# Kernel tuning notes

Hardware: AMD Instinct MI355X
Metric: run time of the kernel (lower is better)

The kernel has to match this reference:

```python
import jax, jax.numpy as jnp
import numpy as np

D = 256          # input_dim (node embedding dim)
ATT_TIMES = 2
ATT_NUM = 2
DIN = D * ATT_NUM  # NTN input dim = 512
F = 16           # feature_map_dim


def setup_inputs() -> dict:
    key = jax.random.key(0)
    ks = jax.random.split(key, 10)
    x1 = jax.random.normal(ks[0], (120000, D), dtype=jnp.float32)
    x2 = jax.random.normal(ks[1], (100000, D), dtype=jnp.float32)
    # attention weight (glorot)
    W0 = jax.random.normal(ks[2], (D, D), dtype=jnp.float32) * (2.0 / (D + D)) ** 0.5
    # NTN params
    V = jax.random.normal(ks[3], (F, 2 * DIN), dtype=jnp.float32) * (2.0 / (F + 2 * DIN)) ** 0.5
    W = jax.random.normal(ks[4], (F, DIN, DIN), dtype=jnp.float32) * (2.0 / (DIN + DIN)) ** 0.5
    b = jax.random.normal(ks[5], (F,), dtype=jnp.float32)
    # projection MLP 16->8->4->2->1, torch Linear weights are (out, in)
    P0 = jax.random.normal(ks[6], (8, 16), dtype=jnp.float32) * (2.0 / (8 + 16)) ** 0.5
    P1 = jax.random.normal(ks[7], (4, 8), dtype=jnp.float32) * (2.0 / (4 + 8)) ** 0.5
    P2 = jax.random.normal(ks[8], (2, 4), dtype=jnp.float32) * (2.0 / (2 + 4)) ** 0.5
    P3 = jax.random.normal(ks[9], (1, 2), dtype=jnp.float32) * (2.0 / (1 + 2)) ** 0.5
    return {"x1": x1, "x2": x2, "W0": W0, "V": V, "W": W, "b": b,
            "P0": P0, "P1": P1, "P2": P2, "P3": P3}


def _attention(x, W0):
    # x: (N, D) -> (1, D*ATT_NUM) graph embedding.
    outs = []
    for _ in range(ATT_NUM):  # 'dot' style: same params each head (eye W), kept for faithfulness
        cur = x
        out = None
        for _ in range(ATT_TIMES):
            temp = jnp.mean(cur, axis=0, keepdims=True)          # (1, D)
            h_avg = jnp.tanh(temp @ W0)                          # att_weight=True
            att = jax.nn.sigmoid(cur @ h_avg.T)                  # (N, 1), W=eye in 'dot' style
            out = att.T @ cur                                    # (1, D)
            cur = cur * att
        outs.append(out)
    return jnp.concatenate(outs, axis=1)                         # (1, DIN)


def _ntn(g1, g2, V, W, b):
    # g1, g2: (1, DIN). Fused bilinear over all F feature maps.
    concat = jnp.concatenate([g1, g2], axis=1)                   # (1, 2*DIN)
    v_term = concat @ V.T                                        # (1, F)
    w_term = jnp.einsum('nd,fde,me->nf', g1, W, g2)              # (1, F)
    return jax.nn.sigmoid(v_term + w_term + b)                   # inneract = sigmoid


def reference(x1, x2, W0, V, W, b, P0, P1, P2, P3):
    g1 = _attention(x1, W0)
    g2 = _attention(x2, W0)
    x = _ntn(g1, g2, V, W, b)                                    # (1, F), branch 'an'
    for P in (P0, P1, P2, P3):                                   # Linear(no bias) + Sigmoid
        x = jax.nn.sigmoid(x @ P.T)
    return x                                                     # (1, 1)
```

## Files before the change

### kernel.cpp

```cpp
#include <hip/hip_runtime.h>
#include <math.h>

#define DD 256
#define REPS 8

#define OFF_SUMREP 0
#define OFF_H1P    4096
#define OFF_S1REP  4608
#define OFF_H2P    8704
#define OFF_OREP   9216
#define OFF_O      13312
#define OFF_WTREP  13824
#define WS_FLOATS  13952

__device__ __forceinline__ float sigmoidf_(float x) { return 1.0f / (1.0f + __expf(-x)); }
__device__ __forceinline__ float dot4(float4 a, float4 b) {
    return a.x * b.x + a.y * b.y + a.z * b.z + a.w * b.w;
}
__device__ __forceinline__ void fma4(float4& acc, float s, float4 v) {
    acc.x += s * v.x; acc.y += s * v.y; acc.z += s * v.z; acc.w += s * v.w;
}
__device__ __forceinline__ float wave_sum(float v) {
#pragma unroll
    for (int off = 32; off; off >>= 1) v += __shfl_xor(v, off, 64);
    return v;
}

__global__ void k_zero(float* __restrict__ ws) {
    int i = blockIdx.x * 256 + threadIdx.x;
    if (i < WS_FLOATS) ws[i] = 0.0f;
}

__device__ __forceinline__ void block_reduce_atomic(float4 acc, int t, float* dst_base) {
    __shared__ float4 lds[256];
    lds[t] = acc;
    __syncthreads();
    if (t < 64) {
        float4 s = lds[t];
        float4 a = lds[t + 64], c = lds[t + 128], d = lds[t + 192];
        s.x += a.x + c.x + d.x; s.y += a.y + c.y + d.y;
        s.z += a.z + c.z + d.z; s.w += a.w + c.w + d.w;
        float* dst = dst_base + t * 4;
        atomicAdd(dst + 0, s.x); atomicAdd(dst + 1, s.y);
        atomicAdd(dst + 2, s.z); atomicAdd(dst + 3, s.w);
    }
}

__global__ void __launch_bounds__(256, 8)
k_mean(const float* __restrict__ x1, const float* __restrict__ x2,
       int N1, int N2, float* __restrict__ ws) {
    int b = blockIdx.x, t = threadIdx.x;
    int inp = b >> 10;
    int bl = b & 1023;
    const float4* x = (const float4*)(inp ? x2 : x1);
    int N = inp ? N2 : N1;
    int chunk = (N + 1023) >> 10;
    int start = bl * chunk;
    int end = min(start + chunk, N);
    int lane = t & 63, w = t >> 6;
    float4 a0 = make_float4(0.f, 0.f, 0.f, 0.f), a1 = a0;
    int r = start + w;
    for (; r + 12 < end; r += 16) {
        const float4* p = x + (size_t)r * 64 + lane;
        float4 v0 = p[0], v1 = p[256], v2 = p[512], v3 = p[768];
        a0.x += v0.x + v1.x; a0.y += v0.y + v1.y; a0.z += v0.z + v1.z; a0.w += v0.w + v1.w;
        a1.x += v2.x + v3.x; a1.y += v2.y + v3.y; a1.z += v2.z + v3.z; a1.w += v2.w + v3.w;
    }
    for (; r < end; r += 4) {
        float4 v = x[(size_t)r * 64 + lane];
        a0.x += v.x; a0.y += v.y; a0.z += v.z; a0.w += v.w;
    }
    a0.x += a1.x; a0.y += a1.y; a0.z += a1.z; a0.w += a1.w;
    block_reduce_atomic(a0, t, ws + OFF_SUMREP + inp * (REPS * 256) + (bl & (REPS - 1)) * 256);
}

__global__ void k_hpart(const float* __restrict__ W0, float* __restrict__ ws,
                        int srcOff, int dstOff, int N1, int N2) {
    int inp = blockIdx.x >> 4, g = blockIdx.x & 15;
    int t = threadIdx.x;
    __shared__ float temp[16];
    if (t < 16) {
        const float* src = ws + srcOff + inp * (REPS * 256) + g * 16 + t;
        float s = 0.f;
#pragma unroll
        for (int r = 0; r < REPS; r++) s += src[r * 256];
        temp[t] = s * (1.0f / (float)(inp ? N2 : N1));
    }
    __syncthreads();
    float p = 0.f;
#pragma unroll
    for (int j = 0; j < 16; j++) p += temp[j] * W0[(g * 16 + j) * 256 + t];
    atomicAdd(ws + dstOff + inp * 256 + t, p);
}

__global__ void __launch_bounds__(256, 8)
k_att1(const float* __restrict__ x1, const float* __restrict__ x2,
       int N1, int N2, float* __restrict__ ws) {
    int b = blockIdx.x, t = threadIdx.x;
    int inp = b >> 10;
    int bl = b & 1023;
    const float4* x = (const float4*)(inp ? x2 : x1);
    int N = inp ? N2 : N1;
    int chunk = (N + 1023) >> 10;
    int start = bl * chunk;
    int end = min(start + chunk, N);
    int lane = t & 63, w = t >> 6;
    float4 hp = ((const float4*)(ws + OFF_H1P + inp * 256))[lane];
    float4 h1 = make_float4(tanhf(hp.x), tanhf(hp.y), tanhf(hp.z), tanhf(hp.w));
    float4 acc = make_float4(0.f, 0.f, 0.f, 0.f);
    int r = start + w;
    for (; r + 12 < end; r += 16) {
        const float4* p = x + (size_t)r * 64 + lane;
        float4 v0 = p[0], v1 = p[256], v2 = p[512], v3 = p[768];
        float d0 = dot4(v0, h1), d1 = dot4(v1, h1), d2 = dot4(v2, h1), d3 = dot4(v3, h1);
#pragma unroll
        for (int off = 32; off; off >>= 1) {
            d0 += __shfl_xor(d0, off, 64); d1 += __shfl_xor(d1, off, 64);
            d2 += __shfl_xor(d2, off, 64); d3 += __shfl_xor(d3, off, 64);
        }
        fma4(acc, sigmoidf_(d0), v0); fma4(acc, sigmoidf_(d1), v1);
        fma4(acc, sigmoidf_(d2), v2); fma4(acc, sigmoidf_(d3), v3);
    }
    for (; r < end; r += 4) {
        float4 v = x[(size_t)r * 64 + lane];
        float d = wave_sum(dot4(v, h1));
        fma4(acc, sigmoidf_(d), v);
    }
    block_reduce_atomic(acc, t, ws + OFF_S1REP + inp * (REPS * 256) + (bl & (REPS - 1)) * 256);
}

__global__ void __launch_bounds__(256, 8)
k_att2(const float* __restrict__ x1, const float* __restrict__ x2,
       int N1, int N2, float* __restrict__ ws) {
    int b = blockIdx.x, t = threadIdx.x;
    int inp = b >> 10;
    int bl = b & 1023;
    const float4* x = (const float4*)(inp ? x2 : x1);
    int N = inp ? N2 : N1;
    int chunk = (N + 1023) >> 10;
    int start = bl * chunk;
    int end = min(start + chunk, N);
    int lane = t & 63, w = t >> 6;
    float4 hp1 = ((const float4*)(ws + OFF_H1P + inp * 256))[lane];
    float4 hp2 = ((const float4*)(ws + OFF_H2P + inp * 256))[lane];
    float4 h1 = make_float4(tanhf(hp1.x), tanhf(hp1.y), tanhf(hp1.z), tanhf(hp1.w));
    float4 h2 = make_float4(tanhf(hp2.x), tanhf(hp2.y), tanhf(hp2.z), tanhf(hp2.w));
    float4 acc = make_float4(0.f, 0.f, 0.f, 0.f);
    int r = start + w;
    for (; r + 12 < end; r += 16) {
        const float4* p = x + (size_t)r * 64 + lane;
        float4 v0 = p[0], v1 = p[256], v2 = p[512], v3 = p[768];
        float d0 = dot4(v0, h1), d1 = dot4(v1, h1), d2 = dot4(v2, h1), d3 = dot4(v3, h1);
        float e0 = dot4(v0, h2), e1 = dot4(v1, h2), e2 = dot4(v2, h2), e3 = dot4(v3, h2);
#pragma unroll
        for (int off = 32; off; off >>= 1) {
            d0 += __shfl_xor(d0, off, 64); e0 += __shfl_xor(e0, off, 64);
            d1 += __shfl_xor(d1, off, 64); e1 += __shfl_xor(e1, off, 64);
            d2 += __shfl_xor(d2, off, 64); e2 += __shfl_xor(e2, off, 64);
            d3 += __shfl_xor(d3, off, 64); e3 += __shfl_xor(e3, off, 64);
        }
        float a1_0 = sigmoidf_(d0), a1_1 = sigmoidf_(d1), a1_2 = sigmoidf_(d2), a1_3 = sigmoidf_(d3);
        fma4(acc, a1_0 * sigmoidf_(a1_0 * e0), v0);
        fma4(acc, a1_1 * sigmoidf_(a1_1 * e1), v1);
        fma4(acc, a1_2 * sigmoidf_(a1_2 * e2), v2);
        fma4(acc, a1_3 * sigmoidf_(a1_3 * e3), v3);
    }
    for (; r < end; r += 4) {
        float4 v = x[(size_t)r * 64 + lane];
        float d = dot4(v, h1), e = dot4(v, h2);
#pragma unroll
        for (int off = 32; off; off >>= 1) {
            d += __shfl_xor(d, off, 64); e += __shfl_xor(e, off, 64);
        }
        float a1 = sigmoidf_(d);
        fma4(acc, a1 * sigmoidf_(a1 * e), v);
    }
    block_reduce_atomic(acc, t, ws + OFF_OREP + inp * (REPS * 256) + (bl & (REPS - 1)) * 256);
}

__global__ void k_comb(float* __restrict__ ws) {
    int t = threadIdx.x;
    int inp = t >> 8, c = t & 255;
    float s = 0.f;
#pragma unroll
    for (int r = 0; r < REPS; r++) s += ws[OFF_OREP + inp * (REPS * 256) + r * 256 + c];
    ws[OFF_O + t] = s;
}

__global__ void __launch_bounds__(256, 8)
k_ntn(const float* __restrict__ W, float* __restrict__ ws) {
    int b = blockIdx.x, t = threadIdx.x;
    int lane = t & 63, w = t >> 6;
    const float* o1 = ws + OFF_O;
    float4 o2f = ((const float4*)(ws + OFF_O + 256))[lane];
    int f = b >> 5;
    int r0 = b * 16 + w;
    const float4* W4 = (const float4*)W;
    float p0, p1, p2, p3;
    {
        const float4* q0 = W4 + (size_t)r0 * 128 + lane;
        float4 a0 = q0[0],   c0 = q0[64];
        float4 a1 = q0[512], c1 = q0[576];
        float4 a2 = q0[1024], c2 = q0[1088];
        float4 a3 = q0[1536], c3 = q0[1600];
        p0 = (a0.x + c0.x) * o2f.x + (a0.y + c0.y) * o2f.y + (a0.z + c0.z) * o2f.z + (a0.w + c0.w) * o2f.w;
        p1 = (a1.x + c1.x) * o2f.x + (a1.y + c1.y) * o2f.y + (a1.z + c1.z) * o2f.z + (a1.w + c1.w) * o2f.w;
        p2 = (a2.x + c2.x) * o2f.x + (a2.y + c2.y) * o2f.y + (a2.z + c2.z) * o2f.z + (a2.w + c2.w) * o2f.w;
        p3 = (a3.x + c3.x) * o2f.x + (a3.y + c3.y) * o2f.y + (a3.z + c3.z) * o2f.z + (a3.w + c3.w) * o2f.w;
    }
#pragma unroll
    for (int off = 32; off; off >>= 1) {
        p0 += __shfl_xor(p0, off, 64); p1 += __shfl_xor(p1, off, 64);
        p2 += __shfl_xor(p2, off, 64); p3 += __shfl_xor(p3, off, 64);
    }
    if (lane == 0) {
        float* dst = ws + OFF_WTREP + (b & (REPS - 1)) * 16 + f;
        int d = r0 & 511;
        atomicAdd(dst, o1[d & 255] * p0
                     + o1[(d + 4) & 255] * p1
                     + o1[(d + 8) & 255] * p2
                     + o1[(d + 12) & 255] * p3);
    }
}

__global__ void k_final(const float* __restrict__ V, const float* __restrict__ bb,
                        const float* __restrict__ P0, const float* __restrict__ P1,
                        const float* __restrict__ P2, const float* __restrict__ P3,
                        float* __restrict__ ws, float* __restrict__ out) {
    int t = threadIdx.x;
    const float* o = ws + OFF_O;
    int f = t >> 4, j = t & 15;
    float p = 0.f;
    for (int k = j; k < 1024; k += 16) {
        float cv = (k < 512) ? o[k & 255] : o[256 + (k & 255)];
        p += cv * V[f * 1024 + k];
    }
    __shared__ float red[256];
    __shared__ float sv[16];
    red[t] = p;
    __syncthreads();
    if (t < 16) {
        float v = 0.f;
#pragma unroll
        for (int q = 0; q < 16; q++) v += red[t * 16 + q];
        float wt = 0.f;
#pragma unroll
        for (int r = 0; r < REPS; r++) wt += ws[OFF_WTREP + r * 16 + t];
        sv[t] = sigmoidf_(v + wt + bb[t]);
    }
    __syncthreads();
    if (t == 0) {
        float y0[8], y1[4], y2[2];
#pragma unroll
        for (int i = 0; i < 8; i++) {
            float s = 0.f;
            for (int k = 0; k < 16; k++) s += P0[i * 16 + k] * sv[k];
            y0[i] = sigmoidf_(s);
        }
#pragma unroll
        for (int i = 0; i < 4; i++) {
            float s = 0.f;
            for (int k = 0; k < 8; k++) s += P1[i * 8 + k] * y0[k];
            y1[i] = sigmoidf_(s);
        }
#pragma unroll
        for (int i = 0; i < 2; i++) {
            float s = 0.f;
            for (int k = 0; k < 4; k++) s += P2[i * 4 + k] * y1[k];
            y2[i] = sigmoidf_(s);
        }
        out[0] = sigmoidf_(P3[0] * y2[0] + P3[1] * y2[1]);
    }
}

extern "C" void kernel_launch(void* const* d_in, const int* in_sizes, int n_in,
                              void* d_out, int out_size, void* d_ws, size_t ws_size,
                              hipStream_t stream) {
    const float* x1 = (const float*)d_in[0];
    const float* x2 = (const float*)d_in[1];
    const float* W0 = (const float*)d_in[2];
    const float* V  = (const float*)d_in[3];
    const float* W  = (const float*)d_in[4];
    const float* b  = (const float*)d_in[5];
    const float* P0 = (const float*)d_in[6];
    const float* P1 = (const float*)d_in[7];
    const float* P2 = (const float*)d_in[8];
    const float* P3 = (const float*)d_in[9];
    float* ws  = (float*)d_ws;
    float* out = (float*)d_out;
    int N1 = in_sizes[0] / DD;
    int N2 = in_sizes[1] / DD;

    k_zero  <<<55,   256, 0, stream>>>(ws);
    k_mean  <<<2048, 256, 0, stream>>>(x1, x2, N1, N2, ws);
    k_hpart <<<32,   256, 0, stream>>>(W0, ws, OFF_SUMREP, OFF_H1P, N1, N2);
    k_att1  <<<2048, 256, 0, stream>>>(x1, x2, N1, N2, ws);
    k_hpart <<<32,   256, 0, stream>>>(W0, ws, OFF_S1REP, OFF_H2P, N1, N2);
    k_att2  <<<2048, 256, 0, stream>>>(x1, x2, N1, N2, ws);
    k_comb  <<<1,    512, 0, stream>>>(ws);
    k_ntn   <<<512,  256, 0, stream>>>(W, ws);
    k_final <<<1,    256, 0, stream>>>(V, b, P0, P1, P2, P3, ws, out);
}
```

Measured before the change: 418.7 us.

## Write fp16 mirror of inputs during mean pass and stream it in attention passes

New measurement: 424.0 us. Within noise of the previous version (+1.3%).

```diff
diff --git a/kernel.cpp b/kernel.cpp
--- a/kernel.cpp
+++ b/kernel.cpp
@@ -9,21 +9,29 @@
 #define OFF_S1REP  4608
 #define OFF_H2P    8704
 #define OFF_OREP   9216
-#define OFF_O      13312
 #define OFF_WTREP  13824
 #define WS_FLOATS  13952
+#define MIRROR_OFF_BYTES 65536
+
+typedef float    f32x4 __attribute__((ext_vector_type(4)));
+typedef _Float16 f16x4 __attribute__((ext_vector_type(4)));
 
 __device__ __forceinline__ float sigmoidf_(float x) { return 1.0f / (1.0f + __expf(-x)); }
-__device__ __forceinline__ float dot4(float4 a, float4 b) {
+__device__ __forceinline__ float dot4(f32x4 a, f32x4 b) {
     return a.x * b.x + a.y * b.y + a.z * b.z + a.w * b.w;
 }
-__device__ __forceinline__ void fma4(float4& acc, float s, float4 v) {
-    acc.x += s * v.x; acc.y += s * v.y; acc.z += s * v.z; acc.w += s * v.w;
+__device__ __forceinline__ f32x4 tanh4(f32x4 a) {
+    f32x4 r; r.x = tanhf(a.x); r.y = tanhf(a.y); r.z = tanhf(a.z); r.w = tanhf(a.w);
+    return r;
 }
 __device__ __forceinline__ float wave_sum(float v) {
 #pragma unroll
     for (int off = 32; off; off >>= 1) v += __shfl_xor(v, off, 64);
     return v;
+}
+__device__ __forceinline__ f32x4 ld4(const f32x4* p, size_t i) { return p[i]; }
+__device__ __forceinline__ f32x4 ld4(const f16x4* p, size_t i) {
+    return __builtin_convertvector(p[i], f32x4);
 }
 
 __global__ void k_zero(float* __restrict__ ws) {
@@ -31,47 +39,53 @@
     if (i < WS_FLOATS) ws[i] = 0.0f;
 }
 
-__device__ __forceinline__ void block_reduce_atomic(float4 acc, int t, float* dst_base) {
-    __shared__ float4 lds[256];
+__device__ __forceinline__ void block_reduce_atomic(f32x4 acc, int t, float* dst_base,
+                                                    f32x4* lds) {
     lds[t] = acc;
     __syncthreads();
     if (t < 64) {
-        float4 s = lds[t];
-        float4 a = lds[t + 64], c = lds[t + 128], d = lds[t + 192];
-        s.x += a.x + c.x + d.x; s.y += a.y + c.y + d.y;
-        s.z += a.z + c.z + d.z; s.w += a.w + c.w + d.w;
+        f32x4 s = lds[t] + lds[t + 64] + lds[t + 128] + lds[t + 192];
         float* dst = dst_base + t * 4;
         atomicAdd(dst + 0, s.x); atomicAdd(dst + 1, s.y);
         atomicAdd(dst + 2, s.z); atomicAdd(dst + 3, s.w);
     }
 }
 
-__global__ void __launch_bounds__(256, 8)
-k_mean(const float* __restrict__ x1, const float* __restrict__ x2,
-       int N1, int N2, float* __restrict__ ws) {
+template<bool WM>
+__global__ void __launch_bounds__(256, 4)
+k_mean_t(const f32x4* __restrict__ x1, const f32x4* __restrict__ x2,
+         f16x4* __restrict__ m1, f16x4* __restrict__ m2,
+         int N1, int N2, float* __restrict__ ws) {
     int b = blockIdx.x, t = threadIdx.x;
-    int inp = b >> 10;
-    int bl = b & 1023;
-    const float4* x = (const float4*)(inp ? x2 : x1);
+    int inp = b >> 10, bl = b & 1023;
+    const f32x4* x = inp ? x2 : x1;
+    f16x4* mm = inp ? m2 : m1;
     int N = inp ? N2 : N1;
     int chunk = (N + 1023) >> 10;
-    int start = bl * chunk;
-    int end = min(start + chunk, N);
+    int start = bl * chunk, end = min(start + chunk, N);
     int lane = t & 63, w = t >> 6;
-    float4 a0 = make_float4(0.f, 0.f, 0.f, 0.f), a1 = a0;
+    f32x4 a0 = {0.f, 0.f, 0.f, 0.f}, a1 = a0;
     int r = start + w;
     for (; r + 12 < end; r += 16) {
-        const float4* p = x + (size_t)r * 64 + lane;
-        float4 v0 = p[0], v1 = p[256], v2 = p[512], v3 = p[768];
-        a0.x += v0.x + v1.x; a0.y += v0.y + v1.y; a0.z += v0.z + v1.z; a0.w += v0.w + v1.w;
-        a1.x += v2.x + v3.x; a1.y += v2.y + v3.y; a1.z += v2.z + v3.z; a1.w += v2.w + v3.w;
+        size_t i0 = (size_t)r * 64 + lane;
+        f32x4 v0 = x[i0], v1 = x[i0 + 256], v2 = x[i0 + 512], v3 = x[i0 + 768];
+        if (WM) {
+            mm[i0]       = __builtin_convertvector(v0, f16x4);
+            mm[i0 + 256] = __builtin_convertvector(v1, f16x4);
+            mm[i0 + 512] = __builtin_convertvector(v2, f16x4);
+            mm[i0 + 768] = __builtin_convertvector(v3, f16x4);
+        }
+        a0 += v0 + v1; a1 += v2 + v3;
     }
     for (; r < end; r += 4) {
-        float4 v = x[(size_t)r * 64 + lane];
-        a0.x += v.x; a0.y += v.y; a0.z += v.z; a0.w += v.w;
-    }
-    a0.x += a1.x; a0.y += a1.y; a0.z += a1.z; a0.w += a1.w;
-    block_reduce_atomic(a0, t, ws + OFF_SUMREP + inp * (REPS * 256) + (bl & (REPS - 1)) * 256);
+        size_t i0 = (size_t)r * 64 + lane;
+        f32x4 v = x[i0];
+        if (WM) mm[i0] = __builtin_convertvector(v, f16x4);
+        a0 += v;
+    }
+    a0 += a1;
+    __shared__ f32x4 lds[256];
+    block_reduce_atomic(a0, t, ws + OFF_SUMREP + inp * (REPS * 256) + (bl & (REPS - 1)) * 256, lds);
 }
 
 __global__ void k_hpart(const float* __restrict__ W0, float* __restrict__ ws,
@@ -93,133 +107,114 @@
     atomicAdd(ws + dstOff + inp * 256 + t, p);
 }
 
-__global__ void __launch_bounds__(256, 8)
-k_att1(const float* __restrict__ x1, const float* __restrict__ x2,
-       int N1, int N2, float* __restrict__ ws) {
+template<typename T>
+__global__ void __launch_bounds__(256, 4)
+k_att1_t(const T* __restrict__ b1, const T* __restrict__ b2,
+         int N1, int N2, float* __restrict__ ws) {
     int b = blockIdx.x, t = threadIdx.x;
-    int inp = b >> 10;
-    int bl = b & 1023;
-    const float4* x = (const float4*)(inp ? x2 : x1);
+    int inp = b >> 10, bl = b & 1023;
+    const T* x = inp ? b2 : b1;
     int N = inp ? N2 : N1;
     int chunk = (N + 1023) >> 10;
-    int start = bl * chunk;
-    int end = min(start + chunk, N);
+    int start = bl * chunk, end = min(start + chunk, N);
     int lane = t & 63, w = t >> 6;
-    float4 hp = ((const float4*)(ws + OFF_H1P + inp * 256))[lane];
-    float4 h1 = make_float4(tanhf(hp.x), tanhf(hp.y), tanhf(hp.z), tanhf(hp.w));
-    float4 acc = make_float4(0.f, 0.f, 0.f, 0.f);
+    f32x4 h1 = tanh4(((const f32x4*)(ws + OFF_H1P + inp * 256))[lane]);
+    f32x4 acc = {0.f, 0.f, 0.f, 0.f};
     int r = start + w;
     for (; r + 12 < end; r += 16) {
-        const float4* p = x + (size_t)r * 64 + lane;
-        float4 v0 = p[0], v1 = p[256], v2 = p[512], v3 = p[768];
+        size_t i0 = (size_t)r * 64 + lane;
+        f32x4 v0 = ld4(x, i0), v1 = ld4(x, i0 + 256), v2 = ld4(x, i0 + 512), v3 = ld4(x, i0 + 768);
         float d0 = dot4(v0, h1), d1 = dot4(v1, h1), d2 = dot4(v2, h1), d3 = dot4(v3, h1);
 #pragma unroll
         for (int off = 32; off; off >>= 1) {
             d0 += __shfl_xor(d0, off, 64); d1 += __shfl_xor(d1, off, 64);
             d2 += __shfl_xor(d2, off, 64); d3 += __shfl_xor(d3, off, 64);
         }
-        fma4(acc, sigmoidf_(d0), v0); fma4(acc, sigmoidf_(d1), v1);
-        fma4(acc, sigmoidf_(d2), v2); fma4(acc, sigmoidf_(d3), v3);
+        acc += sigmoidf_(d0) * v0 + sigmoidf_(d1) * v1;
+        acc += sigmoidf_(d2) * v2 + sigmoidf_(d3) * v3;
     }
     for (; r < end; r += 4) {
-        float4 v = x[(size_t)r * 64 + lane];
-        float d = wave_sum(dot4(v, h1));
-        fma4(acc, sigmoidf_(d), v);
-    }
-    block_reduce_atomic(acc, t, ws + OFF_S1REP + inp * (REPS * 256) + (bl & (REPS - 1)) * 256);
-}
-
-__global__ void __launch_bounds__(256, 8)
-k_att2(const float* __restrict__ x1, const float* __restrict__ x2,
-       int N1, int N2, float* __restrict__ ws) {
+        f32x4 v = ld4(x, (size_t)r * 64 + lane);
+        acc += sigmoidf_(wave_sum(dot4(v, h1))) * v;
+    }
+    __shared__ f32x4 lds[256];
+    block_reduce_atomic(acc, t, ws + OFF_S1REP + inp * (REPS * 256) + (bl & (REPS - 1)) * 256, lds);
+}
+
+template<typename T>
+__global__ void __launch_bounds__(256, 4)
+k_att2_t(const T* __restrict__ b1, const T* __restrict__ b2,
+         int N1, int N2, float* __restrict__ ws) {
     int b = blockIdx.x, t = threadIdx.x;
-    int inp = b >> 10;
-    int bl = b & 1023;
-    const float4* x = (const float4*)(inp ? x2 : x1);
+    int inp = b >> 10, bl = b & 1023;
+    const T* x = inp ? b2 : b1;
     int N = inp ? N2 : N1;
     int chunk = (N + 1023) >> 10;
-    int start = bl * chunk;
-    int end = min(start + chunk, N);
+    int start = bl * chunk, end = min(start + chunk, N);
     int lane = t & 63, w = t >> 6;
-    float4 hp1 = ((const float4*)(ws + OFF_H1P + inp * 256))[lane];
-    float4 hp2 = ((const float4*)(ws + OFF_H2P + inp * 256))[lane];
-    float4 h1 = make_float4(tanhf(hp1.x), tanhf(hp1.y), tanhf(hp1.z), tanhf(hp1.w));
-    float4 h2 = make_float4(tanhf(hp2.x), tanhf(hp2.y), tanhf(hp2.z), tanhf(hp2.w));
-    float4 acc = make_float4(0.f, 0.f, 0.f, 0.f);
+    f32x4 h1 = tanh4(((const f32x4*)(ws + OFF_H1P + inp * 256))[lane]);
+    f32x4 h2 = tanh4(((const f32x4*)(ws + OFF_H2P + inp * 256))[lane]);
+    f32x4 acc = {0.f, 0.f, 0.f, 0.f};
     int r = start + w;
-    for (; r + 12 < end; r += 16) {
-        const float4* p = x + (size_t)r * 64 + lane;
-        float4 v0 = p[0], v1 = p[256], v2 = p[512], v3 = p[768];
-        float d0 = dot4(v0, h1), d1 = dot4(v1, h1), d2 = dot4(v2, h1), d3 = dot4(v3, h1);
-        float e0 = dot4(v0, h2), e1 = dot4(v1, h2), e2 = dot4(v2, h2), e3 = dot4(v3, h2);
+    for (; r + 4 < end; r += 8) {
+        size_t i0 = (size_t)r * 64 + lane;
+        f32x4 v0 = ld4(x, i0), v1 = ld4(x, i0 + 256);
+        float d0 = dot4(v0, h1), d1 = dot4(v1, h1);
+        float e0 = dot4(v0, h2), e1 = dot4(v1, h2);
 #pragma unroll
         for (int off = 32; off; off >>= 1) {
             d0 += __shfl_xor(d0, off, 64); e0 += __shfl_xor(e0, off, 64);
             d1 += __shfl_xor(d1, off, 64); e1 += __shfl_xor(e1, off, 64);
-            d2 += __shfl_xor(d2, off, 64); e2 += __shfl_xor(e2, off, 64);
-            d3 += __shfl_xor(d3, off, 64); e3 += __shfl_xor(e3, off, 64);
-        }
-        float a1_0 = sigmoidf_(d0), a1_1 = sigmoidf_(d1), a1_2 = sigmoidf_(d2), a1_3 = sigmoidf_(d3);
-        fma4(acc, a1_0 * sigmoidf_(a1_0 * e0), v0);
-        fma4(acc, a1_1 * sigmoidf_(a1_1 * e1), v1);
-        fma4(acc, a1_2 * sigmoidf_(a1_2 * e2), v2);
-        fma4(acc, a1_3 * sigmoidf_(a1_3 * e3), v3);
+        }
+        float a0 = sigmoidf_(d0), a1 = sigmoidf_(d1);
+        acc += (a0 * sigmoidf_(a0 * e0)) * v0 + (a1 * sigmoidf_(a1 * e1)) * v1;
     }
     for (; r < end; r += 4) {
-        float4 v = x[(size_t)r * 64 + lane];
+        f32x4 v = ld4(x, (size_t)r * 64 + lane);
         float d = dot4(v, h1), e = dot4(v, h2);
 #pragma unroll
         for (int off = 32; off; off >>= 1) {
             d += __shfl_xor(d, off, 64); e += __shfl_xor(e, off, 64);
         }
         float a1 = sigmoidf_(d);
-        fma4(acc, a1 * sigmoidf_(a1 * e), v);
-    }
-    block_reduce_atomic(acc, t, ws + OFF_OREP + inp * (REPS * 256) + (bl & (REPS - 1)) * 256);
-}
-
-__global__ void k_comb(float* __restrict__ ws) {
-    int t = threadIdx.x;
-    int inp = t >> 8, c = t & 255;
-    float s = 0.f;
-#pragma unroll
-    for (int r = 0; r < REPS; r++) s += ws[OFF_OREP + inp * (REPS * 256) + r * 256 + c];
-    ws[OFF_O + t] = s;
-}
-
-__global__ void __launch_bounds__(256, 8)
+        acc += (a1 * sigmoidf_(a1 * e)) * v;
+    }
+    __shared__ f32x4 lds[256];
+    block_reduce_atomic(acc, t, ws + OFF_OREP + inp * (REPS * 256) + (bl & (REPS - 1)) * 256, lds);
+}
+
+__global__ void __launch_bounds__(256, 4)
 k_ntn(const float* __restrict__ W, float* __restrict__ ws) {
+    __shared__ __align__(16) float o_l[512];
     int b = blockIdx.x, t = threadIdx.x;
+    {
+        float s0 = 0.f, s1 = 0.f;
+#pragma unroll
+        for (int r2 = 0; r2 < REPS; r2++) {
+            s0 += ws[OFF_OREP + r2 * 256 + t];
+            s1 += ws[OFF_OREP + REPS * 256 + r2 * 256 + t];
+        }
+        o_l[t] = s0; o_l[256 + t] = s1;
+    }
+    __syncthreads();
     int lane = t & 63, w = t >> 6;
-    const float* o1 = ws + OFF_O;
-    float4 o2f = ((const float4*)(ws + OFF_O + 256))[lane];
-    int f = b >> 5;
-    int r0 = b * 16 + w;
-    const float4* W4 = (const float4*)W;
-    float p0, p1, p2, p3;
-    {
-        const float4* q0 = W4 + (size_t)r0 * 128 + lane;
-        float4 a0 = q0[0],   c0 = q0[64];
-        float4 a1 = q0[512], c1 = q0[576];
-        float4 a2 = q0[1024], c2 = q0[1088];
-        float4 a3 = q0[1536], c3 = q0[1600];
-        p0 = (a0.x + c0.x) * o2f.x + (a0.y + c0.y) * o2f.y + (a0.z + c0.z) * o2f.z + (a0.w + c0.w) * o2f.w;
-        p1 = (a1.x + c1.x) * o2f.x + (a1.y + c1.y) * o2f.y + (a1.z + c1.z) * o2f.z + (a1.w + c1.w) * o2f.w;
-        p2 = (a2.x + c2.x) * o2f.x + (a2.y + c2.y) * o2f.y + (a2.z + c2.z) * o2f.z + (a2.w + c2.w) * o2f.w;
-        p3 = (a3.x + c3.x) * o2f.x + (a3.y + c3.y) * o2f.y + (a3.z + c3.z) * o2f.z + (a3.w + c3.w) * o2f.w;
-    }
-#pragma unroll
-    for (int off = 32; off; off >>= 1) {
-        p0 += __shfl_xor(p0, off, 64); p1 += __shfl_xor(p1, off, 64);
-        p2 += __shfl_xor(p2, off, 64); p3 += __shfl_xor(p3, off, 64);
+    f32x4 o2f = ((const f32x4*)(o_l + 256))[lane];
+    int g = b * 4 + w;
+    const f32x4* W4 = (const f32x4*)W;
+    float wt[4];
+    int fidx[4];
+#pragma unroll
+    for (int u = 0; u < 4; u++) {
+        int row = g + u * 2048;
+        const f32x4* q = W4 + (size_t)row * 128 + lane;
+        float p = wave_sum(dot4(q[0] + q[64], o2f));
+        wt[u] = o_l[row & 255] * p;
+        fidx[u] = row >> 9;
     }
     if (lane == 0) {
-        float* dst = ws + OFF_WTREP + (b & (REPS - 1)) * 16 + f;
-        int d = r0 & 511;
-        atomicAdd(dst, o1[d & 255] * p0
-                     + o1[(d + 4) & 255] * p1
-                     + o1[(d + 8) & 255] * p2
-                     + o1[(d + 12) & 255] * p3);
+        float* dst = ws + OFF_WTREP + (b & (REPS - 1)) * 16;
+#pragma unroll
+        for (int u = 0; u < 4; u++) atomicAdd(dst + fidx[u], wt[u]);
     }
 }
 
@@ -228,11 +223,21 @@
                         const float* __restrict__ P2, const float* __restrict__ P3,
                         float* __restrict__ ws, float* __restrict__ out) {
     int t = threadIdx.x;
-    const float* o = ws + OFF_O;
+    __shared__ float o_l[512];
+    {
+        float s0 = 0.f, s1 = 0.f;
+#pragma unroll
+        for (int r2 = 0; r2 < REPS; r2++) {
+            s0 += ws[OFF_OREP + r2 * 256 + t];
+            s1 += ws[OFF_OREP + REPS * 256 + r2 * 256 + t];
+        }
+        o_l[t] = s0; o_l[256 + t] = s1;
+    }
+    __syncthreads();
     int f = t >> 4, j = t & 15;
     float p = 0.f;
     for (int k = j; k < 1024; k += 16) {
-        float cv = (k < 512) ? o[k & 255] : o[256 + (k & 255)];
+        float cv = (k < 512) ? o_l[k & 255] : o_l[256 + (k & 255)];
         p += cv * V[f * 1024 + k];
     }
     __shared__ float red[256];
@@ -291,13 +296,27 @@
     int N1 = in_sizes[0] / DD;
     int N2 = in_sizes[1] / DD;
 
-    k_zero  <<<55,   256, 0, stream>>>(ws);
-    k_mean  <<<2048, 256, 0, stream>>>(x1, x2, N1, N2, ws);
-    k_hpart <<<32,   256, 0, stream>>>(W0, ws, OFF_SUMREP, OFF_H1P, N1, N2);
-    k_att1  <<<2048, 256, 0, stream>>>(x1, x2, N1, N2, ws);
-    k_hpart <<<32,   256, 0, stream>>>(W0, ws, OFF_S1REP, OFF_H2P, N1, N2);
-    k_att2  <<<2048, 256, 0, stream>>>(x1, x2, N1, N2, ws);
-    k_comb  <<<1,    512, 0, stream>>>(ws);
-    k_ntn   <<<512,  256, 0, stream>>>(W, ws);
-    k_final <<<1,    256, 0, stream>>>(V, b, P0, P1, P2, P3, ws, out);
-}
+    const f32x4* x1v = (const f32x4*)x1;
+    const f32x4* x2v = (const f32x4*)x2;
+    f16x4* m1 = (f16x4*)((char*)d_ws + MIRROR_OFF_BYTES);
+    f16x4* m2 = m1 + (size_t)N1 * 64;
+    size_t need = (size_t)MIRROR_OFF_BYTES + ((size_t)N1 + N2) * DD * sizeof(_Float16);
+    bool use_mirror = ws_size >= need;
+
+    k_zero <<<55, 256, 0, stream>>>(ws);
+    if (use_mirror) {
+        k_mean_t<true>  <<<2048, 256, 0, stream>>>(x1v, x2v, m1, m2, N1, N2, ws);
+        k_hpart         <<<32,   256, 0, stream>>>(W0, ws, OFF_SUMREP, OFF_H1P, N1, N2);
+        k_att1_t<f16x4> <<<2048, 256, 0, stream>>>(m1, m2, N1, N2, ws);
+        k_hpart         <<<32,   256, 0, stream>>>(W0, ws, OFF_S1REP, OFF_H2P, N1, N2);
+        k_att2_t<f16x4> <<<2048, 256, 0, stream>>>(m1, m2, N1, N2, ws);
+    } else {
+        k_mean_t<false> <<<2048, 256, 0, stream>>>(x1v, x2v, nullptr, nullptr, N1, N2, ws);
+        k_hpart         <<<32,   256, 0, stream>>>(W0, ws, OFF_SUMREP, OFF_H1P, N1, N2);
+        k_att1_t<f32x4> <<<2048, 256, 0, stream>>>(x1v, x2v, N1, N2, ws);
+        k_hpart         <<<32,   256, 0, stream>>>(W0, ws, OFF_S1REP, OFF_H2P, N1, N2);
+        k_att2_t<f32x4> <<<2048, 256, 0, stream>>>(x1v, x2v, N1, N2, ws);
+    }
+    k_ntn  <<<512, 256, 0, stream>>>(W, ws);
+    k_final<<<1,   256, 0, stream>>>(V, b, P0, P1, P2, P3, ws, out);
+}
```
